# Optimization experiments

Hardware: AMD Instinct MI355X
Metric: run time of the kernel (lower is better)

The kernel has to match this reference:

```python
import jax, jax.numpy as jnp
import numpy as np

N, E = 20000, 320000          # nodes, edges (avg in-degree ~16)
F_IN, EMB, T, OUT = 40, 40, 5, 2
F_T = EMB // T                # per-tower output width = 8
EPS_STD, EPS_GN = 1e-5, 1e-5


def _lin_init(k, fan_in, fan_out, extra=()):
    return jax.random.normal(k, (*extra, fan_in, fan_out), jnp.float32) / np.sqrt(fan_in)


def setup_inputs() -> dict:
    key = jax.random.key(0)
    ks = jax.random.split(key, 8)
    # deg histogram in init: all 20000 nodes with degree 16 -> avg_deg['log'] = log(16+1)
    return dict(
        x=jax.random.normal(ks[0], (N, F_IN), jnp.float32),
        edge_index=jax.random.randint(ks[1], (2, E), 0, N),
        W_pre=_lin_init(ks[2], 2 * F_IN, F_IN, (T,)),   # per-tower pre-MLP
        b_pre=jnp.zeros((T, F_IN), jnp.float32),
        W_post=_lin_init(ks[3], 13 * F_IN, F_T, (T,)),  # (4 agg * 3 scalers + 1 residual) * F_in
        b_post=jnp.zeros((T, F_T), jnp.float32),
        W_lin=_lin_init(ks[4], T * F_T, EMB),           # PNAConv final mixing linear
        b_lin=jnp.zeros((EMB,), jnp.float32),
        gn_weight=jnp.ones((EMB,), jnp.float32),
        gn_bias=jnp.zeros((EMB,), jnp.float32),
        gn_mean_scale=jnp.ones((EMB,), jnp.float32),
        W1=_lin_init(ks[5], EMB, EMB),                  # head hidden linear
        b1=jnp.zeros((EMB,), jnp.float32),
        W2=_lin_init(ks[6], EMB, OUT),                  # head output linear
        b2=jnp.zeros((OUT,), jnp.float32),
        avg_deg_log=jnp.float32(np.log(17.0)),
    )


def _pna_conv(x, src, dst, W_pre, b_pre, W_post, b_post, W_lin, b_lin, avg_deg_log):
    xi, xj = x[dst], x[src]                              # gather: [E, F]
    h = jnp.concatenate([xi, xj], axis=-1)               # [E, 2F]
    m = jnp.einsum('ef,tfg->etg', h, W_pre) + b_pre      # per-tower messages [E, T, F]
    cnt = jax.ops.segment_sum(jnp.ones((E,), m.dtype), dst, num_segments=N)  # in-degree [N]
    denom = jnp.maximum(cnt, 1.0)[:, None, None]
    mean = jax.ops.segment_sum(m, dst, num_segments=N) / denom
    mean2 = jax.ops.segment_sum(m * m, dst, num_segments=N) / denom
    std = jnp.sqrt(jax.nn.relu(mean2 - mean * mean) + EPS_STD)
    has = (cnt > 0)[:, None, None]
    mn = jnp.where(has, jax.ops.segment_min(m, dst, num_segments=N), 0.0)
    mx = jnp.where(has, jax.ops.segment_max(m, dst, num_segments=N), 0.0)
    agg = jnp.concatenate([mean, mn, mx, std], axis=-1)  # [N, T, 4F]
    deg = jnp.maximum(cnt, 1.0)[:, None, None]
    logd = jnp.log(deg + 1.0)
    out = jnp.concatenate(
        [agg, agg * (logd / avg_deg_log), agg * (avg_deg_log / logd)], axis=-1)  # [N, T, 12F]
    out = jnp.concatenate(
        [jnp.broadcast_to(x[:, None, :], (N, T, x.shape[-1])), out], axis=-1)    # [N, T, 13F]
    out = jnp.einsum('ntf,tfg->ntg', out, W_post) + b_post                       # [N, T, F_T]
    return out.reshape(N, T * F_T) @ W_lin + b_lin


def _graph_norm(x, w, b, mean_scale):
    mean = jnp.mean(x, axis=0, keepdims=True)
    out = x - mean_scale * mean
    var = jnp.mean(out * out, axis=0, keepdims=True)
    return w * out / jnp.sqrt(var + EPS_GN) + b


def reference(x, edge_index, W_pre, b_pre, W_post, b_post, W_lin, b_lin,
              gn_weight, gn_bias, gn_mean_scale, W1, b1, W2, b2, avg_deg_log):
    src, dst = edge_index[0], edge_index[1]
    h = _pna_conv(x, src, dst, W_pre, b_pre, W_post, b_post, W_lin, b_lin, avg_deg_log)
    h = jax.nn.relu(_graph_norm(h, gn_weight, gn_bias, gn_mean_scale))
    h = jax.nn.relu(h @ W1 + b1)   # dropout_rate=None -> no dropout
    return h @ W2 + b2
```

## Files before the change

kernel.cpp:

```cpp
#include <hip/hip_runtime.h>
#include <math.h>

#define N_NODES 20000
#define N_EDGES 320000
#define F_IN 40
#define T_TOW 5
#define EMB 40
#define NPB_PRE 16
#define NBLK_MIX 313
#define NBLK_PM 313
#define ECHUNK 16
#define STRIDE 64

typedef __attribute__((ext_vector_type(8))) _Float16 half8;
typedef __attribute__((ext_vector_type(2))) _Float16 half2_t;
typedef __attribute__((ext_vector_type(4))) float f32x4;

#define WS_STATS   0
#define WS_CURSOR  320
#define WS_SSRC    80384
#define WS_MS      5200384
#define WS_MD      13200384
#define WS_AGG     21200384
#define WS_XPOST   53200384
#define WS_H0T     69200384
#define WS_PART    72400384

__global__ __launch_bounds__(256) void k_pre(const float* __restrict__ x,
                                             const float* __restrict__ W_pre,
                                             const float* __restrict__ b_pre,
                                             const float* __restrict__ W_post,
                                             const float* __restrict__ b_post,
                                             _Float16* __restrict__ mS,
                                             _Float16* __restrict__ mD,
                                             float* __restrict__ xpostT,
                                             int* __restrict__ cursor) {
  const int tid = threadIdx.x;
  const int n0 = blockIdx.x * NPB_PRE;
  if (tid < NPB_PRE) cursor[n0 + tid] = (n0 + tid) * STRIDE;
  const bool statlane = tid < 200;
  const int q = tid - 200;
  const bool xplane = (q >= 0 && q < 40);
  const int tc = statlane ? tid : 199;
  const int t = tc / 40, g = tc - t * 40;
  const int t2 = xplane ? q / 8 : 0, g2 = xplane ? q - (q / 8) * 8 : 0;
  float wA[40], wB[40];
  const float* Wt = W_pre + t * 3200;
#pragma unroll
  for (int j = 0; j < 40; ++j) {
    wA[j] = statlane ? Wt[j * 40 + g] : W_post[t2 * 4160 + j * 8 + g2];
    wB[j] = statlane ? Wt[(40 + j) * 40 + g] : 0.f;
  }
  const float bias = statlane ? b_pre[t * 40 + g] : b_post[t2 * 8 + g2];
  for (int ni = 0; ni < NPB_PRE; ++ni) {
    const int n = n0 + ni;
    const float* xr = x + n * F_IN;
    float aA = bias, aB = 0.f;
#pragma unroll
    for (int j = 0; j < 40; j += 4) {
      const float4 xv = *(const float4*)(xr + j);
      aA += xv.x * wA[j] + xv.y * wA[j + 1] + xv.z * wA[j + 2] + xv.w * wA[j + 3];
      aB += xv.x * wB[j] + xv.y * wB[j + 1] + xv.z * wB[j + 2] + xv.w * wB[j + 3];
    }
    if (statlane) {
      mD[n * 200 + tc] = (_Float16)aA;
      mS[n * 200 + tc] = (_Float16)aB;
    } else if (xplane) {
      xpostT[t2 * (N_NODES * 8) + n * 8 + g2] = aA;
    }
  }
}

__global__ __launch_bounds__(256) void k_scatter(const int* __restrict__ src,
                                                 const int* __restrict__ dst,
                                                 int* __restrict__ cursor,
                                                 int* __restrict__ ssrc) {
  int i = blockIdx.x * 256 + threadIdx.x;
  if (i < N_EDGES) {
    int d = dst[i];
    int pos = atomicAdd(&cursor[d], 1);
    ssrc[pos] = src[i];
  }
}

__global__ __launch_bounds__(256) void k_edge(const _Float16* __restrict__ mS,
                                              const _Float16* __restrict__ mD,
                                              const int* __restrict__ cursor,
                                              const int* __restrict__ ssrc,
                                              _Float16* __restrict__ aggS) {
  const int lane = threadIdx.x & 63;
  const int wv = threadIdx.x >> 6;
  const int n = blockIdx.x * 4 + wv;
  const int r0 = n * STRIDE;
  const int r1 = __builtin_amdgcn_readfirstlane(cursor[n]);
  const int cnt = r1 - r0;
  const int myidx = ssrc[r0 + lane];
  const int cpa = lane;
  const bool bact = lane < 36;
  const int cpb = bact ? 64 + lane : 99;
  const half2_t mda = ((const half2_t*)(mD + n * 200))[cpa];
  const half2_t mdb = ((const half2_t*)(mD + n * 200))[cpb];

  const _Float16 HINF = (_Float16)65504.f;
  half2_t suma = {0, 0}, ssqa = {0, 0}, sumb = {0, 0}, ssqb = {0, 0};
  half2_t mna = {HINF, HINF}, mxa = {-HINF, -HINF};
  half2_t mnb = {HINF, HINF}, mxb = {-HINF, -HINF};
  half2_t va = {0, 0}, vb = {0, 0};

  if (cnt > 0) {
    for (int p = 0; p < cnt; p += ECHUNK) {
      half2_t ha[ECHUNK], hb[ECHUNK];
#pragma unroll
      for (int i = 0; i < ECHUNK; ++i) {
        const int ii = (p + i < cnt) ? (p + i) : (cnt - 1);
        const int s = __builtin_amdgcn_readlane(myidx, ii);
        const half2_t* row = (const half2_t*)(mS + s * 200);
        ha[i] = row[cpa];
        hb[i] = row[cpb];
      }
#pragma unroll
      for (int i = 0; i < ECHUNK; ++i) {
        suma += ha[i];
        ssqa += ha[i] * ha[i];
        mna = __builtin_elementwise_min(mna, ha[i]);
        mxa = __builtin_elementwise_max(mxa, ha[i]);
        sumb += hb[i];
        ssqb += hb[i] * hb[i];
        mnb = __builtin_elementwise_min(mnb, hb[i]);
        mxb = __builtin_elementwise_max(mxb, hb[i]);
      }
      va = ha[ECHUNK - 1];
      vb = hb[ECHUNK - 1];
    }
  }

  const int padded = ((cnt + ECHUNK - 1) / ECHUNK) * ECHUNK;
  const float d = (float)(padded - cnt);
  const float inv = (cnt > 0) ? 1.f / (float)cnt : 0.f;
#pragma unroll
  for (int set = 0; set < 2; ++set) {
    if (set == 1 && !bact) break;
    const int cp = set == 0 ? cpa : cpb;
    const half2_t sum2 = set == 0 ? suma : sumb;
    const half2_t ssq2 = set == 0 ? ssqa : ssqb;
    const half2_t mn2 = set == 0 ? mna : mnb;
    const half2_t mx2 = set == 0 ? mxa : mxb;
    const half2_t vl2 = set == 0 ? va : vb;
    const half2_t md2 = set == 0 ? mda : mdb;
    half2_t omean, omn, omx, osd;
#pragma unroll
    for (int j = 0; j < 2; ++j) {
      float mean, mnf, mxf, sd;
      if (cnt > 0) {
        const float vl = (float)vl2[j];
        const float sf = (float)sum2[j] - d * vl;
        const float qf = (float)ssq2[j] - d * vl * vl;
        const float msm = sf * inv;
        const float var = qf * inv - msm * msm;
        sd = sqrtf(fmaxf(var, 0.f) + 1e-5f);
        const float mdf = (float)md2[j];
        mean = mdf + msm;
        mnf = mdf + (float)mn2[j];
        mxf = mdf + (float)mx2[j];
      } else {
        mean = 0.f; mnf = 0.f; mxf = 0.f; sd = sqrtf(1e-5f);
      }
      omean[j] = (_Float16)mean;
      omn[j] = (_Float16)mnf;
      omx[j] = (_Float16)mxf;
      osd[j] = (_Float16)sd;
    }
    const int t = cp / 20, g = 2 * (cp - t * 20);
    _Float16* abase = aggS + ((size_t)t * N_NODES + n) * 160 + g;
    *(half2_t*)(abase) = omean;
    *(half2_t*)(abase + 40) = omn;
    *(half2_t*)(abase + 80) = omx;
    *(half2_t*)(abase + 120) = osd;
  }
}

__global__ __launch_bounds__(320) void k_postmix(const _Float16* __restrict__ aggT,
                                                 const int* __restrict__ cursor,
                                                 const float* __restrict__ W_post,
                                                 const float* __restrict__ avg_dl,
                                                 const float* __restrict__ xpostT,
                                                 const float* __restrict__ W_lin,
                                                 const float* __restrict__ b_lin,
                                                 float* __restrict__ h0T,
                                                 float* __restrict__ partial) {
  __shared__ float sP[64 * 41];
  const int tid = threadIdx.x;
  const int t = tid >> 6;
  const int l = tid & 63;
  const int n0 = blockIdx.x * 64;
  const int c = l & 15;
  const int kg = l >> 4;

  const float* Wt = W_post + t * 4160;
  half8 b1f[5], b2f[5];
#pragma unroll
  for (int ks = 0; ks < 5; ++ks) {
#pragma unroll
    for (int j = 0; j < 8; ++j) {
      const int k = ks * 32 + kg * 8 + j;
      const float w1v = (c < 8) ? Wt[(40 + k) * 8 + c] : Wt[(200 + k) * 8 + (c - 8)];
      const float w2v = (c < 8) ? Wt[(360 + k) * 8 + c] : 0.f;
      b1f[ks][j] = (_Float16)w1v;
      b2f[ks][j] = (_Float16)w2v;
    }
  }
  const float avg = avg_dl[0];

  for (int tile = 0; tile < 4; ++tile) {
    const int nb = n0 + tile * 16;
    int nA = nb + c;
    if (nA >= N_NODES) nA = N_NODES - 1;
    const half8* ar = (const half8*)(aggT + ((size_t)t * N_NODES + nA) * 160);
    half8 af[5];
#pragma unroll
    for (int ks = 0; ks < 5; ++ks) af[ks] = ar[ks * 4 + kg];
    f32x4 acc1 = {0.f, 0.f, 0.f, 0.f}, acc2 = {0.f, 0.f, 0.f, 0.f};
#pragma unroll
    for (int ks = 0; ks < 5; ++ks) {
      acc1 = __builtin_amdgcn_mfma_f32_16x16x32_f16(af[ks], b1f[ks], acc1, 0, 0, 0);
      acc2 = __builtin_amdgcn_mfma_f32_16x16x32_f16(af[ks], b2f[ks], acc2, 0, 0, 0);
    }
    float bp[4];
#pragma unroll
    for (int r = 0; r < 4; ++r) bp[r] = __shfl_xor(acc1[r], 8, 64);
    if (c < 8) {
#pragma unroll
      for (int r = 0; r < 4; ++r) {
        const int nn0 = nb + kg * 4 + r;
        const int nn = (nn0 < N_NODES) ? nn0 : N_NODES - 1;
        const int cnt = cursor[nn] - nn * STRIDE;
        const float ld = logf(fmaxf((float)cnt, 1.f) + 1.f);
        const float s1 = ld / avg, s2 = avg / ld;
        const float xp = xpostT[t * (N_NODES * 8) + nn * 8 + c];
        sP[(tile * 16 + kg * 4 + r) * 41 + t * 8 + c] =
            acc1[r] + s1 * bp[r] + s2 * acc2[r] + xp;
      }
    }
  }
  __syncthreads();

  const int c0 = t * 8;
  float acc[8];
#pragma unroll
  for (int j = 0; j < 8; ++j) acc[j] = b_lin[c0 + j];
  for (int k = 0; k < 40; ++k) {
    const float p = sP[l * 41 + k];
    const float* w = W_lin + k * EMB + c0;
#pragma unroll
    for (int j = 0; j < 8; ++j) acc[j] = fmaf(p, w[j], acc[j]);
  }
  const int n = n0 + l;
  const bool ok = n < N_NODES;
  if (ok) {
#pragma unroll
    for (int j = 0; j < 8; ++j) h0T[(c0 + j) * N_NODES + n] = acc[j];
  }
#pragma unroll
  for (int j = 0; j < 8; ++j) {
    float sv = ok ? acc[j] : 0.f;
    float qv = sv * sv;
#pragma unroll
    for (int m = 32; m >= 1; m >>= 1) {
      sv += __shfl_xor(sv, m, 64);
      qv += __shfl_xor(qv, m, 64);
    }
    if (l == 0) {
      partial[blockIdx.x * 80 + c0 + j] = sv;
      partial[blockIdx.x * 80 + 40 + c0 + j] = qv;
    }
  }
}

__global__ __launch_bounds__(256) void k_stats(const float* __restrict__ partial,
                                               float* __restrict__ S1,
                                               float* __restrict__ S2) {
  const int col = blockIdx.x;
  const int tid = threadIdx.x;
  __shared__ float red[4];
  float s = 0.f;
  for (int b = tid; b < NBLK_PM; b += 256) s += partial[b * 80 + col];
#pragma unroll
  for (int m = 32; m >= 1; m >>= 1) s += __shfl_xor(s, m, 64);
  if ((tid & 63) == 0) red[tid >> 6] = s;
  __syncthreads();
  if (tid == 0) {
    const float tot = (red[0] + red[1]) + (red[2] + red[3]);
    if (col < 40) S1[col] = tot;
    else S2[col - 40] = tot;
  }
}

__global__ __launch_bounds__(256) void k_head(const float* __restrict__ S1,
                                              const float* __restrict__ S2,
                                              const float* __restrict__ h0T,
                                              const float* __restrict__ gn_w,
                                              const float* __restrict__ gn_b,
                                              const float* __restrict__ gn_ms,
                                              const float* __restrict__ W1,
                                              const float* __restrict__ b1,
                                              const float* __restrict__ W2,
                                              const float* __restrict__ b2,
                                              float* __restrict__ out) {
  __shared__ float sV[64 * 41];
  __shared__ float sH[64 * 41];
  const int tid = threadIdx.x;
  const int n0 = blockIdx.x * 64;
  const float invN = 1.f / (float)N_NODES;
  for (int i = 0; i < 10; ++i) {
    const int idx = tid + i * 256;
    const int e = idx >> 6, r = idx & 63;
    const int nn0 = n0 + r;
    const int nn = (nn0 < N_NODES) ? nn0 : 0;
    const float M = S1[e] * invN;
    const float ms = gn_ms[e];
    const float var = S2[e] * invN - ms * (2.f - ms) * M * M;
    const float sc = gn_w[e] / sqrtf(var + 1e-5f);
    const float he = h0T[e * N_NODES + nn];
    sV[r * 41 + e] = fmaxf((he - ms * M) * sc + gn_b[e], 0.f);
  }
  __syncthreads();
  const int wv = tid >> 6, lane = tid & 63;
  const int c0 = wv * 10;
  float acc[10];
#pragma unroll
  for (int j = 0; j < 10; ++j) acc[j] = b1[c0 + j];
  for (int k = 0; k < 40; ++k) {
    const float p = sV[lane * 41 + k];
    const float* w = W1 + k * EMB + c0;
#pragma unroll
    for (int j = 0; j < 10; ++j) acc[j] = fmaf(p, w[j], acc[j]);
  }
#pragma unroll
  for (int j = 0; j < 10; ++j) sH[lane * 41 + c0 + j] = fmaxf(acc[j], 0.f);
  __syncthreads();
  if (tid < 64) {
    const int n = n0 + tid;
    if (n < N_NODES) {
      float o0 = b2[0], o1 = b2[1];
      const float* hr = sH + tid * 41;
#pragma unroll
      for (int k = 0; k < 40; ++k) {
        const float r = hr[k];
        o0 = fmaf(r, W2[k * 2], o0);
        o1 = fmaf(r, W2[k * 2 + 1], o1);
      }
      out[n * 2] = o0;
      out[n * 2 + 1] = o1;
    }
  }
}

extern "C" void kernel_launch(void* const* d_in, const int* in_sizes, int n_in,
                              void* d_out, int out_size, void* d_ws, size_t ws_size,
                              hipStream_t stream) {
  const float* x      = (const float*)d_in[0];
  const int*   ei     = (const int*)d_in[1];
  const float* W_pre  = (const float*)d_in[2];
  const float* b_pre  = (const float*)d_in[3];
  const float* W_post = (const float*)d_in[4];
  const float* b_post = (const float*)d_in[5];
  const float* W_lin  = (const float*)d_in[6];
  const float* b_lin  = (const float*)d_in[7];
  const float* gn_w   = (const float*)d_in[8];
  const float* gn_b   = (const float*)d_in[9];
  const float* gn_ms  = (const float*)d_in[10];
  const float* W1     = (const float*)d_in[11];
  const float* b1     = (const float*)d_in[12];
  const float* W2     = (const float*)d_in[13];
  const float* b2     = (const float*)d_in[14];
  const float* avg_dl = (const float*)d_in[15];
  float* out = (float*)d_out;

  char* ws = (char*)d_ws;
  float* S1   = (float*)(ws + WS_STATS);
  float* S2   = S1 + 40;
  int* cursor = (int*)(ws + WS_CURSOR);
  int* ssrc   = (int*)(ws + WS_SSRC);
  _Float16* mS   = (_Float16*)(ws + WS_MS);
  _Float16* mD   = (_Float16*)(ws + WS_MD);
  _Float16* aggS = (_Float16*)(ws + WS_AGG);
  float* xpostT  = (float*)(ws + WS_XPOST);
  float* h0T     = (float*)(ws + WS_H0T);
  float* part    = (float*)(ws + WS_PART);
  const int* e_src = ei;
  const int* e_dst = ei + N_EDGES;

  k_pre<<<N_NODES / NPB_PRE, 256, 0, stream>>>(x, W_pre, b_pre, W_post, b_post,
                                               mS, mD, xpostT, cursor);
  k_scatter<<<(N_EDGES + 255) / 256, 256, 0, stream>>>(e_src, e_dst, cursor, ssrc);
  k_edge<<<N_NODES / 4, 256, 0, stream>>>(mS, mD, cursor, ssrc, aggS);
  k_postmix<<<NBLK_PM, 320, 0, stream>>>(aggS, cursor, W_post, avg_dl,
                                         xpostT, W_lin, b_lin, h0T, part);
  k_stats<<<80, 256, 0, stream>>>(part, S1, S2);
  k_head<<<NBLK_MIX, 256, 0, stream>>>(S1, S2, h0T, gn_w, gn_b, gn_ms,
                                       W1, b1, W2, b2, out);
}
```

Baseline: 194.5 us.

## Pad per-node cursors to separate cache lines and halve postmix block size

Measured after the change: 195.5 us. Within noise of the previous version (+0.5%).

```diff
diff --git a/kernel.cpp b/kernel.cpp
--- a/kernel.cpp
+++ b/kernel.cpp
@@ -8,9 +8,10 @@
 #define EMB 40
 #define NPB_PRE 16
 #define NBLK_MIX 313
-#define NBLK_PM 313
+#define NBLK_PM 625
 #define ECHUNK 16
 #define STRIDE 64
+#define CPAD 16
 
 typedef __attribute__((ext_vector_type(8))) _Float16 half8;
 typedef __attribute__((ext_vector_type(2))) _Float16 half2_t;
@@ -18,13 +19,13 @@
 
 #define WS_STATS   0
 #define WS_CURSOR  320
-#define WS_SSRC    80384
-#define WS_MS      5200384
-#define WS_MD      13200384
-#define WS_AGG     21200384
-#define WS_XPOST   53200384
-#define WS_H0T     69200384
-#define WS_PART    72400384
+#define WS_SSRC    1280384
+#define WS_MS      6400384
+#define WS_MD      14400384
+#define WS_AGG     22400384
+#define WS_XPOST   54400384
+#define WS_H0T     57600384
+#define WS_PART    60800384
 
 __global__ __launch_bounds__(256) void k_pre(const float* __restrict__ x,
                                              const float* __restrict__ W_pre,
@@ -37,7 +38,7 @@
                                              int* __restrict__ cursor) {
   const int tid = threadIdx.x;
   const int n0 = blockIdx.x * NPB_PRE;
-  if (tid < NPB_PRE) cursor[n0 + tid] = (n0 + tid) * STRIDE;
+  if (tid < NPB_PRE) cursor[(n0 + tid) * CPAD] = (n0 + tid) * STRIDE;
   const bool statlane = tid < 200;
   const int q = tid - 200;
   const bool xplane = (q >= 0 && q < 40);
@@ -78,7 +79,7 @@
   int i = blockIdx.x * 256 + threadIdx.x;
   if (i < N_EDGES) {
     int d = dst[i];
-    int pos = atomicAdd(&cursor[d], 1);
+    int pos = atomicAdd(&cursor[d * CPAD], 1);
     ssrc[pos] = src[i];
   }
 }
@@ -92,7 +93,7 @@
   const int wv = threadIdx.x >> 6;
   const int n = blockIdx.x * 4 + wv;
   const int r0 = n * STRIDE;
-  const int r1 = __builtin_amdgcn_readfirstlane(cursor[n]);
+  const int r1 = __builtin_amdgcn_readfirstlane(cursor[n * CPAD]);
   const int cnt = r1 - r0;
   const int myidx = ssrc[r0 + lane];
   const int cpa = lane;
@@ -188,11 +189,11 @@
                                                  const float* __restrict__ b_lin,
                                                  float* __restrict__ h0T,
                                                  float* __restrict__ partial) {
-  __shared__ float sP[64 * 41];
+  __shared__ float sP[32 * 41];
   const int tid = threadIdx.x;
   const int t = tid >> 6;
   const int l = tid & 63;
-  const int n0 = blockIdx.x * 64;
+  const int n0 = blockIdx.x * 32;
   const int c = l & 15;
   const int kg = l >> 4;
 
@@ -211,10 +212,9 @@
   }
   const float avg = avg_dl[0];
 
-  for (int tile = 0; tile < 4; ++tile) {
+  for (int tile = 0; tile < 2; ++tile) {
     const int nb = n0 + tile * 16;
-    int nA = nb + c;
-    if (nA >= N_NODES) nA = N_NODES - 1;
+    const int nA = nb + c;
     const half8* ar = (const half8*)(aggT + ((size_t)t * N_NODES + nA) * 160);
     half8 af[5];
 #pragma unroll
@@ -231,9 +231,8 @@
     if (c < 8) {
 #pragma unroll
       for (int r = 0; r < 4; ++r) {
-        const int nn0 = nb + kg * 4 + r;
-        const int nn = (nn0 < N_NODES) ? nn0 : N_NODES - 1;
-        const int cnt = cursor[nn] - nn * STRIDE;
+        const int nn = nb + kg * 4 + r;
+        const int cnt = cursor[nn * CPAD] - nn * STRIDE;
         const float ld = logf(fmaxf((float)cnt, 1.f) + 1.f);
         const float s1 = ld / avg, s2 = avg / ld;
         const float xp = xpostT[t * (N_NODES * 8) + nn * 8 + c];
@@ -244,34 +243,34 @@
   }
   __syncthreads();
 
-  const int c0 = t * 8;
-  float acc[8];
-#pragma unroll
-  for (int j = 0; j < 8; ++j) acc[j] = b_lin[c0 + j];
+  const int nb = l & 31;
+  const int ch = l >> 5;
+  const int cc = t * 8 + ch * 4;
+  const float4 bb = *(const float4*)(b_lin + cc);
+  float acc[4] = {bb.x, bb.y, bb.z, bb.w};
   for (int k = 0; k < 40; ++k) {
-    const float p = sP[l * 41 + k];
-    const float* w = W_lin + k * EMB + c0;
-#pragma unroll
-    for (int j = 0; j < 8; ++j) acc[j] = fmaf(p, w[j], acc[j]);
-  }
-  const int n = n0 + l;
-  const bool ok = n < N_NODES;
-  if (ok) {
-#pragma unroll
-    for (int j = 0; j < 8; ++j) h0T[(c0 + j) * N_NODES + n] = acc[j];
-  }
-#pragma unroll
-  for (int j = 0; j < 8; ++j) {
-    float sv = ok ? acc[j] : 0.f;
-    float qv = sv * sv;
-#pragma unroll
-    for (int m = 32; m >= 1; m >>= 1) {
+    const float p = sP[nb * 41 + k];
+    const float4 w = *(const float4*)(W_lin + k * EMB + cc);
+    acc[0] = fmaf(p, w.x, acc[0]);
+    acc[1] = fmaf(p, w.y, acc[1]);
+    acc[2] = fmaf(p, w.z, acc[2]);
+    acc[3] = fmaf(p, w.w, acc[3]);
+  }
+  const int n = n0 + nb;
+#pragma unroll
+  for (int j = 0; j < 4; ++j) h0T[(cc + j) * N_NODES + n] = acc[j];
+#pragma unroll
+  for (int j = 0; j < 4; ++j) {
+    float sv = acc[j];
+    float qv = acc[j] * acc[j];
+#pragma unroll
+    for (int m = 1; m <= 16; m <<= 1) {
       sv += __shfl_xor(sv, m, 64);
       qv += __shfl_xor(qv, m, 64);
     }
-    if (l == 0) {
-      partial[blockIdx.x * 80 + c0 + j] = sv;
-      partial[blockIdx.x * 80 + 40 + c0 + j] = qv;
+    if (nb == 0) {
+      partial[blockIdx.x * 80 + cc + j] = sv;
+      partial[blockIdx.x * 80 + 40 + cc + j] = qv;
     }
   }
 }
```
